# Optimization experiments

Hardware: AMD Instinct MI355X
Metric: run time of the kernel (lower is better)

The kernel has to match this reference:

```python
import jax, jax.numpy as jnp
import numpy as np
import math

N_FILT = 512
FILT_DIM = 1025
BATCH = 64
FS = 16000.0
FFT_N = 512  # hard-coded n=512 in the original np.fft.rfft call


def setup_inputs() -> dict:
    key = jax.random.key(0)
    kq, = jax.random.split(key, 1)
    # Q factors: positive, realistic filter quality factors in [2, 10)
    Q = jax.random.uniform(kq, (BATCH, N_FILT), dtype=jnp.float32) * 8.0 + 2.0
    # center frequencies exactly as the module computes f_cos:
    # fdelta = fs/2/N_filt; fc = arange(fdelta/2, fs/2, fdelta)
    fdelta = FS / 2.0 / N_FILT
    fc = jnp.asarray(np.arange(fdelta / 2.0, FS / 2.0, fdelta), dtype=jnp.float32)
    return {"Q": Q, "fc": fc}


def reference(Q, fc):
    # Q: [B, F] quality factors, fc: [F] center frequencies (Hz)
    T = FILT_DIM - 1
    # nT = t_right * fs = [1, 2, ..., N-1]
    n = jnp.arange(1, T + 1, dtype=Q.dtype)                      # [T]
    BW = fc[None, :] / Q                                         # [B, F]
    alpha = BW * (0.5 * math.sqrt(2.0 * math.pi))                # [B, F]
    b = alpha / FS                                               # [B, F]
    omega_c = (2.0 * math.pi / FS) * fc                          # [F]
    # y[b,f,t] = exp(-(b*n)^2) * cos(omega_c * n)
    env = jnp.exp(-jnp.square(b[:, :, None] * n))                # [B, F, T]
    carrier = jnp.cos(omega_c[None, :, None] * n)                # [1, F, T] bcast
    y = env * carrier                                            # [B, F, T]
    # per-filter max |rfft| over batch and frequency bins (detached in original)
    fft_mag = jnp.abs(jnp.fft.rfft(y, n=FFT_N, axis=-1))         # [B, F, 257]
    maxfft = jax.lax.stop_gradient(jnp.max(fft_mag, axis=(0, 2)))  # [F]
    filters = jnp.flip(y / maxfft[None, :, None], axis=-1)       # [B, F, T]
    return filters
```

## Files before the change

kernel.cpp:

```cpp
#include <hip/hip_runtime.h>


#define BCOEF_K 7.8332133582218756e-05f
#define INV_FS  6.25e-05f
#define TWO_PI  6.28318530717958647692f
#define PI_F    3.14159265358979323846f
#define SIGK_K  115.2309f

typedef float vf4 __attribute__((ext_vector_type(4)));

__device__ __forceinline__ float fast_carrier(float fcn, float n) {
  float rev = fcn * n;
  float fr  = rev - floorf(rev);
  return __cosf(TWO_PI * fr);
}

__device__ __forceinline__ float fast_env(float x) { return __expf(-x * x); }

__global__ __launch_bounds__(256) void k_maxfft(const float* __restrict__ Q,
                                                const float* __restrict__ fc,
                                                float* __restrict__ maxsq) {
  const int tid  = threadIdx.x;
  const int w    = tid >> 6;
  const int lane = tid & 63;
  const int sig  = blockIdx.x * 4 + w;
  const int f    = sig & 511;
  const int bb   = sig >> 9;

  __shared__ __align__(16) float ybuf[4][512];

  const float fcv = fc[f];
  const float q   = Q[bb * 512 + f];
  const float bc  = (fcv / q) * BCOEF_K;
  const float fcn = fcv * INV_FS;

  const float nstar = 4.0f / bc;
  const int   N_eff = (nstar >= 510.0f) ? 512 : ((int)nstar + 2);
  const int   jmax  = (N_eff + 3) >> 2;

  if (8 * lane < 4 * jmax) {
    float v[8];
    #pragma unroll
    for (int m = 0; m < 8; ++m) {
      const float n = (float)(8 * lane + m + 1);
      v[m] = fast_env(bc * n) * fast_carrier(fcn, n);
    }
    float* yw = &ybuf[w][0];
    ((float4*)(yw + 8 * lane))[0] = make_float4(v[0], v[1], v[2], v[3]);
    ((float4*)(yw + 8 * lane))[1] = make_float4(v[4], v[5], v[6], v[7]);
  }
  __syncthreads();

  const float kc   = fcn * 512.0f;
  const int   kci  = (int)(kc + 0.5f);
  const int   W    = (int)(2.0f * (bc * SIGK_K)) + 6;
  const int   k_lo = max(0, kci - W);
  const int   k_hi = min(256, kci + W);
  const int   nit  = ((k_hi - k_lo) >> 6) + 1;

  const float4* y4 = (const float4*)&ybuf[w][0];
  float mx = 0.0f;

  for (int it = 0; it < nit; ++it) {
    const int   k = min(k_lo + (it << 6) + lane, k_hi);
    const float c = 2.0f * cosf((float)k * (PI_F / 256.0f));
    float s1 = 0.0f, s2 = 0.0f;
    #pragma unroll 4
    for (int j = 0; j < jmax; ++j) {
      const float4 x = y4[j];
      float s;
      s = fmaf(c, s1, x.x - s2); s2 = s1; s1 = s;
      s = fmaf(c, s1, x.y - s2); s2 = s1; s1 = s;
      s = fmaf(c, s1, x.z - s2); s2 = s1; s1 = s;
      s = fmaf(c, s1, x.w - s2); s2 = s1; s1 = s;
    }
    mx = fmaxf(mx, fmaf(s1, s1, fmaf(s2, s2, -(c * s1 * s2))));
  }

  #pragma unroll
  for (int d = 32; d > 0; d >>= 1) mx = fmaxf(mx, __shfl_xor(mx, d));
  if (lane == 0) {
    atomicMax((int*)(maxsq + f), __float_as_int(mx));
  }
}

__global__ __launch_bounds__(256) void k_write(const float* __restrict__ Q,
                                               const float* __restrict__ fc,
                                               const float* __restrict__ maxsq,
                                               float* __restrict__ out) {
  const int blk = blockIdx.x;
  const int f   = blk & 511;
  const int bb  = blk >> 9;
  const int tid = threadIdx.x;

  const float fcv = fc[f];
  const float q   = Q[bb * 512 + f];
  const float bc  = (fcv / q) * BCOEF_K;
  const float fcn = fcv * INV_FS;
  const float nstar = 4.0f / bc;

  const int t0 = tid * 4;
  vf4 r = {0.0f, 0.0f, 0.0f, 0.0f};
  if ((float)(1021 - t0) <= nstar) {
    const float inv = rsqrtf(maxsq[f]);
    const float n0 = (float)(1024 - t0);
    const float n1 = (float)(1023 - t0);
    const float n2 = (float)(1022 - t0);
    const float n3 = (float)(1021 - t0);
    r.x = fast_env(bc * n0) * fast_carrier(fcn, n0) * inv;
    r.y = fast_env(bc * n1) * fast_carrier(fcn, n1) * inv;
    r.z = fast_env(bc * n2) * fast_carrier(fcn, n2) * inv;
    r.w = fast_env(bc * n3) * fast_carrier(fcn, n3) * inv;
  }
  __builtin_nontemporal_store(r, &((vf4*)out)[blk * 256 + tid]);
}

extern "C" void kernel_launch(void* const* d_in, const int* in_sizes, int n_in,
                              void* d_out, int out_size, void* d_ws, size_t ws_size,
                              hipStream_t stream) {
  const float* Q  = (const float*)d_in[0];
  const float* fc = (const float*)d_in[1];
  float* out      = (float*)d_out;
  float* maxsq    = (float*)d_ws;

  (void)hipMemsetAsync(maxsq, 0, 512 * sizeof(float), stream);

  k_maxfft<<<64 * 512 / 4, 256, 0, stream>>>(Q, fc, maxsq);
  k_write <<<64 * 512,     256, 0, stream>>>(Q, fc, maxsq, out);
}
```

Before: 172.6 us.

## Drop atomics and memset, use fixed 64-bin window, wave-local sync

The per-filter max is no longer reduced with atomicMax into a memset buffer. Each signal now writes its partial max to a [F,64] workspace, and the write kernel reduces those 64 values with shuffles, which removes the memset launch and the atomics. The Goertzel search now covers a fixed 64-bin window centred on the carrier bin, one bin per lane, instead of an adaptive window that could need several passes. The block barrier is replaced by an LDS waitcnt, since each wave only reads its own buffer. The fixed window assumes the spectral peak always lies within about 31 bins of the carrier, and the buffer fill now strides per lane rather than writing 8 contiguous values per lane.

```diff
diff --git a/kernel.cpp b/kernel.cpp
--- a/kernel.cpp
+++ b/kernel.cpp
@@ -5,7 +5,6 @@
 #define INV_FS  6.25e-05f
 #define TWO_PI  6.28318530717958647692f
 #define PI_F    3.14159265358979323846f
-#define SIGK_K  115.2309f
 
 typedef float vf4 __attribute__((ext_vector_type(4)));
 
@@ -19,7 +18,7 @@
 
 __global__ __launch_bounds__(256) void k_maxfft(const float* __restrict__ Q,
                                                 const float* __restrict__ fc,
-                                                float* __restrict__ maxsq) {
+                                                float* __restrict__ ws) {
   const int tid  = threadIdx.x;
   const int w    = tid >> 6;
   const int lane = tid & 63;
@@ -37,61 +36,52 @@
   const float nstar = 4.0f / bc;
   const int   N_eff = (nstar >= 510.0f) ? 512 : ((int)nstar + 2);
   const int   jmax  = (N_eff + 3) >> 2;
+  const int   n4    = jmax << 2;
 
-  if (8 * lane < 4 * jmax) {
-    float v[8];
-    #pragma unroll
-    for (int m = 0; m < 8; ++m) {
-      const float n = (float)(8 * lane + m + 1);
-      v[m] = fast_env(bc * n) * fast_carrier(fcn, n);
-    }
-    float* yw = &ybuf[w][0];
-    ((float4*)(yw + 8 * lane))[0] = make_float4(v[0], v[1], v[2], v[3]);
-    ((float4*)(yw + 8 * lane))[1] = make_float4(v[4], v[5], v[6], v[7]);
+  float* yw = &ybuf[w][0];
+  const int nit_g = (n4 + 63) >> 6;
+  for (int r = 0; r < nit_g; ++r) {
+    const int idx = (r << 6) + lane;
+    const float n = (float)(idx + 1);
+    const float v = fast_env(bc * n) * fast_carrier(fcn, n);
+    if (idx < n4) yw[idx] = v;
   }
-  __syncthreads();
+  asm volatile("s_waitcnt lgkmcnt(0)" ::: "memory");
 
-  const float kc   = fcn * 512.0f;
-  const int   kci  = (int)(kc + 0.5f);
-  const int   W    = (int)(2.0f * (bc * SIGK_K)) + 6;
-  const int   k_lo = max(0, kci - W);
-  const int   k_hi = min(256, kci + W);
-  const int   nit  = ((k_hi - k_lo) >> 6) + 1;
+  const int kci = (int)(fcn * 512.0f + 0.5f);
+  const int k   = min(max(kci - 31 + lane, 0), 256);
+  const float c = 2.0f * cosf((float)k * (PI_F / 256.0f));
 
-  const float4* y4 = (const float4*)&ybuf[w][0];
-  float mx = 0.0f;
-
-  for (int it = 0; it < nit; ++it) {
-    const int   k = min(k_lo + (it << 6) + lane, k_hi);
-    const float c = 2.0f * cosf((float)k * (PI_F / 256.0f));
-    float s1 = 0.0f, s2 = 0.0f;
-    #pragma unroll 4
-    for (int j = 0; j < jmax; ++j) {
-      const float4 x = y4[j];
-      float s;
-      s = fmaf(c, s1, x.x - s2); s2 = s1; s1 = s;
-      s = fmaf(c, s1, x.y - s2); s2 = s1; s1 = s;
-      s = fmaf(c, s1, x.z - s2); s2 = s1; s1 = s;
-      s = fmaf(c, s1, x.w - s2); s2 = s1; s1 = s;
-    }
-    mx = fmaxf(mx, fmaf(s1, s1, fmaf(s2, s2, -(c * s1 * s2))));
+  float s1 = 0.0f, s2 = 0.0f;
+  const float4* y4 = (const float4*)yw;
+  #pragma unroll 4
+  for (int j = 0; j < jmax; ++j) {
+    const float4 x = y4[j];
+    float s;
+    s = fmaf(c, s1, x.x - s2); s2 = s1; s1 = s;
+    s = fmaf(c, s1, x.y - s2); s2 = s1; s1 = s;
+    s = fmaf(c, s1, x.z - s2); s2 = s1; s1 = s;
+    s = fmaf(c, s1, x.w - s2); s2 = s1; s1 = s;
   }
+  float mx = fmaf(s1, s1, fmaf(s2, s2, -(c * s1 * s2)));
 
   #pragma unroll
   for (int d = 32; d > 0; d >>= 1) mx = fmaxf(mx, __shfl_xor(mx, d));
-  if (lane == 0) {
-    atomicMax((int*)(maxsq + f), __float_as_int(mx));
-  }
+  if (lane == 0) ws[f * 64 + bb] = mx;
 }
 
 __global__ __launch_bounds__(256) void k_write(const float* __restrict__ Q,
                                                const float* __restrict__ fc,
-                                               const float* __restrict__ maxsq,
+                                               const float* __restrict__ ws,
                                                float* __restrict__ out) {
   const int blk = blockIdx.x;
   const int f   = blk & 511;
   const int bb  = blk >> 9;
   const int tid = threadIdx.x;
+
+  float mx = ws[f * 64 + (tid & 63)];
+  #pragma unroll
+  for (int d = 32; d > 0; d >>= 1) mx = fmaxf(mx, __shfl_xor(mx, d));
 
   const float fcv = fc[f];
   const float q   = Q[bb * 512 + f];
@@ -102,7 +92,7 @@
   const int t0 = tid * 4;
   vf4 r = {0.0f, 0.0f, 0.0f, 0.0f};
   if ((float)(1021 - t0) <= nstar) {
-    const float inv = rsqrtf(maxsq[f]);
+    const float inv = rsqrtf(mx);
     const float n0 = (float)(1024 - t0);
     const float n1 = (float)(1023 - t0);
     const float n2 = (float)(1022 - t0);
@@ -121,10 +111,8 @@
   const float* Q  = (const float*)d_in[0];
   const float* fc = (const float*)d_in[1];
   float* out      = (float*)d_out;
-  float* maxsq    = (float*)d_ws;
+  float* ws       = (float*)d_ws;
 
-  (void)hipMemsetAsync(maxsq, 0, 512 * sizeof(float), stream);
-
-  k_maxfft<<<64 * 512 / 4, 256, 0, stream>>>(Q, fc, maxsq);
-  k_write <<<64 * 512,     256, 0, stream>>>(Q, fc, maxsq, out);
+  k_maxfft<<<64 * 512 / 4, 256, 0, stream>>>(Q, fc, ws);
+  k_write <<<64 * 512,     256, 0, stream>>>(Q, fc, ws, out);
 }
```

Result: faster. 164.7 us (-4.6%).
